# Optimization experiments

Hardware: AMD Instinct MI355X
Metric: run time of the kernel (lower is better)

Reference implementation:

```python
import jax, jax.numpy as jnp
import numpy as np

EPS = 1e-5  # BatchNorm1d default eps


def _knn_idx(coords, k):
    # squared pairwise distances via gram trick (monotone in cdist, same topk order)
    sq = jnp.sum(coords * coords, axis=-1)                     # [B,N]
    d2 = sq[:, :, None] + sq[:, None, :] - 2.0 * jnp.einsum('bnd,bmd->bnm', coords, coords)
    _, idx = jax.lax.top_k(-d2, k)                             # smallest distances
    return idx                                                  # [B,N,k]


def _shared_mlp(x, W, b, gamma, beta):
    # Linear -> BatchNorm1d (training-mode batch stats over B,N per channel) -> ReLU
    y = x @ W + b                                              # [B,N,C]
    m = jnp.mean(y, axis=(0, 1))
    v = jnp.var(y, axis=(0, 1))                                # biased, as torch BN
    y = (y - m) / jnp.sqrt(v + EPS) * gamma + beta
    return jax.nn.relu(y)


def setup_inputs() -> dict:
    key = jax.random.key(0)
    ks = jax.random.split(key, 16)
    B, N, in_ch, out_ch, k = 4, 8192, 64, 128, 16
    mid = out_ch // 2
    s = 0.05
    inp = {
        'coords': jax.random.normal(ks[0], (B, N, 3), jnp.float32),
        'feats': jax.random.normal(ks[1], (B, N, in_ch), jnp.float32),
        'k': k,
        'W1': jax.random.normal(ks[2], (in_ch, mid), jnp.float32) * s,
        'b1': jnp.zeros((mid,), jnp.float32),
        'g1': jnp.ones((mid,), jnp.float32),
        'be1': jnp.zeros((mid,), jnp.float32),
        'Wa': jax.random.normal(ks[3], (mid, mid), jnp.float32) * s,
        'ba': jnp.zeros((mid,), jnp.float32),
        'ga': jnp.ones((mid,), jnp.float32),
        'bea': jnp.zeros((mid,), jnp.float32),
        'W2': jax.random.normal(ks[4], (mid, out_ch), jnp.float32) * s,
        'b2': jnp.zeros((out_ch,), jnp.float32),
        'g2': jnp.ones((out_ch,), jnp.float32),
        'be2': jnp.zeros((out_ch,), jnp.float32),
    }
    return inp


def reference(coords, feats, k, W1, b1, g1, be1, Wa, ba, ga, bea, W2, b2, g2, be2):
    B, N, _ = coords.shape
    idx = _knn_idx(coords, k)                                  # [B,N,k]
    # gather neighbor features: feats[b, idx[b,n,j]]
    neighbors = feats[jnp.arange(B)[:, None, None], idx]       # [B,N,k,C_in]
    agg = _shared_mlp(neighbors.mean(axis=2), W1, b1, g1, be1) # [B,N,mid]
    attn = jax.nn.sigmoid(_shared_mlp(agg, Wa, ba, ga, bea))
    fused = agg * attn + agg
    return _shared_mlp(fused, W2, b2, g2, be2)                 # [B,N,out_ch]
```

## Files before the change

### kernel.cpp

```cpp
#include <hip/hip_runtime.h>
#include <hip/hip_bf16.h>
#include <hip/hip_fp16.h>
#include <math.h>

#define B_ 4
#define N_ 8192
#define K_ 16
#define BN_ (B_ * N_)
#define EPS_ 1e-5f

#define KW_ 8
#define KT_ (KW_ * 64)
#define MCAND (N_ / KW_)
#define SAMP 256
#define DEPTH 8

#define NBLK 512
#define ROWS 64

#define KEY_SENTINEL 0x7F800000FFFFFFFFULL

__global__ __launch_bounds__(256) void pack_coords(const float* __restrict__ coords,
                                                   float4* __restrict__ out) {
    int i = blockIdx.x * 256 + threadIdx.x;
    if (i >= BN_) return;
    out[i] = make_float4(coords[3 * i], coords[3 * i + 1], coords[3 * i + 2], 0.0f);
}

__global__ __launch_bounds__(256) void feats2h(const float* __restrict__ in,
                                               __half* __restrict__ outh) {
    int i = blockIdx.x * 256 + threadIdx.x;
    const float4* p = (const float4*)(in + (size_t)i * 8);
    float4 a = p[0], b = p[1];
    __half2 h0; h0.x = __float2half_rn(a.x); h0.y = __float2half_rn(a.y);
    __half2 h1; h1.x = __float2half_rn(a.z); h1.y = __float2half_rn(a.w);
    __half2 h2; h2.x = __float2half_rn(b.x); h2.y = __float2half_rn(b.y);
    __half2 h3; h3.x = __float2half_rn(b.z); h3.y = __float2half_rn(b.w);
    uint4 o;
    o.x = *(unsigned*)&h0; o.y = *(unsigned*)&h1; o.z = *(unsigned*)&h2; o.w = *(unsigned*)&h3;
    ((uint4*)outh)[i] = o;
}

__global__ __launch_bounds__(KT_) void knn_2ph(const float4* __restrict__ coords4,
                                               int* __restrict__ idxOut) {
    __shared__ unsigned long long bufp[DEPTH][KT_];
    __shared__ unsigned long long accs[KW_][64];

    int t = threadIdx.x;
    int lane = t & 63;
    int w = __builtin_amdgcn_readfirstlane(t >> 6);
    int b = blockIdx.x >> 7;
    int g = blockIdx.x & 127;

    const float4* cb = coords4 + (size_t)b * N_;
    int q = g * 64 + lane;
    float4 qc = cb[q];
    float qx = qc.x, qy = qc.y, qz = qc.z;

    const int base = w * MCAND;

    unsigned long long acc = 0;
    for (int i = 0; i < SAMP; i += 8) {
        float4 c0 = cb[base + i + 0];
        float4 c1 = cb[base + i + 1];
        float4 c2 = cb[base + i + 2];
        float4 c3 = cb[base + i + 3];
        float4 c4 = cb[base + i + 4];
        float4 c5 = cb[base + i + 5];
        float4 c6 = cb[base + i + 6];
        float4 c7 = cb[base + i + 7];
#define H1(cv)                                                         \
        {                                                              \
            float dx = qx - cv.x, dy = qy - cv.y, dz = qz - cv.z;      \
            float d2 = dx * dx;                                        \
            d2 = fmaf(dy, dy, d2);                                     \
            d2 = fmaf(dz, dz, d2);                                     \
            int e = (int)(__float_as_uint(d2) >> 23);                  \
            int bk = (e - 118) >> 1;                                   \
            bk = bk < 0 ? 0 : (bk > 7 ? 7 : bk);                       \
            acc += 1ULL << (bk << 3);                                  \
        }
        H1(c0) H1(c1) H1(c2) H1(c3) H1(c4) H1(c5) H1(c6) H1(c7)
#undef H1
    }
    accs[w][lane] = acc;
    __syncthreads();

    float T;
    {
        const unsigned long long M8 = 0x00FF00FF00FF00FFULL;
        unsigned long long se = 0, so = 0;
#pragma unroll
        for (int ww = 0; ww < KW_; ++ww) {
            unsigned long long a = accs[ww][lane];
            se += a & M8;
            so += (a >> 8) & M8;
        }
        int cum = 0;
        int B = 8;
#pragma unroll
        for (int bb = 0; bb < 8; ++bb) {
            unsigned long long s = (bb & 1) ? so : se;
            int c = (int)((s >> ((bb >> 1) << 4)) & 0xFFFF);
            cum += c;
            if (cum >= K_ && B == 8) B = bb;
        }
        T = (B >= 7) ? 3.4e38f : __uint_as_float((unsigned)(118 + 2 * B + 2) << 23);
    }

    unsigned long long key[K_];
#pragma unroll
    for (int j = 0; j < K_; j++) key[j] = KEY_SENTINEL;

    int cnt = 0;
    float limf = T;

    auto flush = [&]() {
        for (int j = 0; j < cnt; ++j) {
            unsigned long long e = bufp[j][t];
            if (e < key[K_ - 1]) {
#pragma unroll
                for (int jj = K_ - 1; jj > 0; --jj) {
                    bool up = e < key[jj - 1];
                    unsigned long long lo = (e < key[jj]) ? e : key[jj];
                    key[jj] = up ? key[jj - 1] : lo;
                }
                if (e < key[0]) key[0] = e;
            }
        }
        cnt = 0;
        float own = __uint_as_float((unsigned)(key[K_ - 1] >> 32));
        limf = fminf(own, T);
    };

    for (int i = 0; i < MCAND; i += 8) {
        float4 c0 = cb[base + i + 0];
        float4 c1 = cb[base + i + 1];
        float4 c2 = cb[base + i + 2];
        float4 c3 = cb[base + i + 3];
        float4 c4 = cb[base + i + 4];
        float4 c5 = cb[base + i + 5];
        float4 c6 = cb[base + i + 6];
        float4 c7 = cb[base + i + 7];
#define P2(cv, mm)                                                     \
        {                                                              \
            float dx = qx - cv.x, dy = qy - cv.y, dz = qz - cv.z;      \
            float d2 = dx * dx;                                        \
            d2 = fmaf(dy, dy, d2);                                     \
            d2 = fmaf(dz, dz, d2);                                     \
            if (d2 <= limf) {                                          \
                bufp[cnt][t] = ((unsigned long long)__float_as_uint(d2) << 32) | \
                               (unsigned)(mm);                         \
                cnt++;                                                 \
            }                                                          \
        }
        P2(c0, base + i + 0) P2(c1, base + i + 1) P2(c2, base + i + 2) P2(c3, base + i + 3)
        if (__any(cnt >= DEPTH - 3)) flush();
        P2(c4, base + i + 4) P2(c5, base + i + 5) P2(c6, base + i + 6) P2(c7, base + i + 7)
#undef P2
        if (__any(cnt >= DEPTH - 3)) flush();
    }
    flush();

    for (int step = 1; step < KW_; step <<= 1) {
        bool active = (w & (2 * step - 1)) == 0;
        int pb = t + step * 64;
        __syncthreads();
#pragma unroll
        for (int j = 0; j < 8; j++) bufp[j][t] = key[j];
        __syncthreads();
        if (active) {
#pragma unroll
            for (int i = 8; i < 16; i++) {
                unsigned long long o = bufp[15 - i][pb];
                key[i] = key[i] < o ? key[i] : o;
            }
        }
        __syncthreads();
#pragma unroll
        for (int j = 0; j < 8; j++) bufp[j][t] = key[8 + j];
        __syncthreads();
        if (active) {
#pragma unroll
            for (int i = 0; i < 8; i++) {
                unsigned long long o = bufp[7 - i][pb];
                key[i] = key[i] < o ? key[i] : o;
            }
#pragma unroll
            for (int s = 8; s >= 1; s >>= 1) {
#pragma unroll
                for (int i = 0; i < 16; i++) {
                    if ((i & s) == 0) {
                        unsigned long long a = key[i], c = key[i | s];
                        key[i] = a < c ? a : c;
                        key[i | s] = a < c ? c : a;
                    }
                }
            }
        }
    }

    if (w == 0) {
        int* op = idxOut + ((size_t)b * N_ + q) * K_;
#pragma unroll
        for (int r2 = 0; r2 < K_; ++r2) op[r2] = (int)(key[r2] & 0xFFFFFFFFu);
    }
}

__global__ __launch_bounds__(512) void g1_kernel(const __half* __restrict__ fh,
                                                 const int* __restrict__ idx,
                                                 const float* __restrict__ W1,
                                                 const float* __restrict__ b1,
                                                 float* __restrict__ Y1,
                                                 float* __restrict__ part1) {
    __shared__ float buf[ROWS][65];
    int t = threadIdx.x;
    int rl = t & 63;
    int h2 = __builtin_amdgcn_readfirstlane(t >> 6);
    int vbid = ((blockIdx.x & 7) << 6) + (blockIdx.x >> 3);
    int row = vbid * ROWS + rl;
    int bb = row >> 13;

    const __half* fb = fh + ((size_t)bb << 13) * 64;
    const int* ip = idx + (size_t)row * K_;

    float xh[8];
#pragma unroll
    for (int j = 0; j < 8; j++) xh[j] = 0.0f;
#pragma unroll
    for (int j = 0; j < K_; j++) {
        uint4 a = *(const uint4*)(fb + (((size_t)ip[j]) << 6) + h2 * 8);
        __half2* hp = (__half2*)&a;
#pragma unroll
        for (int p = 0; p < 4; p++) {
            float2 f = __half22float2(hp[p]);
            xh[2 * p] += f.x;
            xh[2 * p + 1] += f.y;
        }
    }
#pragma unroll
    for (int j = 0; j < 8; j++) buf[rl][h2 * 8 + j] = xh[j] * (1.0f / 16.0f);
    __syncthreads();

    float acc[8];
#pragma unroll
    for (int j = 0; j < 8; j++) acc[j] = b1[h2 * 8 + j];
#pragma unroll 1
    for (int c0 = 0; c0 < 64; c0 += 16) {
        float xr[16];
#pragma unroll
        for (int j = 0; j < 16; j++) xr[j] = buf[rl][c0 + j];
#pragma unroll
        for (int cc = 0; cc < 16; cc++) {
            float xv = xr[cc];
            const float* wr = W1 + (c0 + cc) * 64 + h2 * 8;
#pragma unroll
            for (int j = 0; j < 8; j++) acc[j] = fmaf(xv, wr[j], acc[j]);
        }
    }
    float2* yp = (float2*)(Y1 + (size_t)row * 64 + h2 * 8);
#pragma unroll
    for (int f = 0; f < 4; f++) yp[f] = make_float2(acc[2 * f], acc[2 * f + 1]);
    __syncthreads();
#pragma unroll
    for (int j = 0; j < 8; j++) buf[rl][h2 * 8 + j] = acc[j];
    __syncthreads();
    if (t < 128) {
        int c = t & 63;
        float s = 0.0f;
        if (t < 64) { for (int r = 0; r < ROWS; ++r) s += buf[r][c]; }
        else        { for (int r = 0; r < ROWS; ++r) { float v = buf[r][c]; s = fmaf(v, v, s); } }
        part1[blockIdx.x * 128 + t] = s;
    }
}

__device__ __forceinline__ void reduce_stats64(const float* __restrict__ part,
                                               const float* __restrict__ gma,
                                               const float* __restrict__ bta,
                                               float* red4, float* scs, float* shs) {
    int t = threadIdx.x;
    {
        int c = t & 127;
        int q = t >> 7;
        float s = 0.0f;
#pragma unroll 8
        for (int g = q * 128; g < q * 128 + 128; ++g) s += part[(size_t)g * 128 + c];
        red4[t] = s;
    }
    __syncthreads();
    if (t < 128) red4[t] = red4[t] + red4[t + 128] + red4[t + 256] + red4[t + 384];
    __syncthreads();
    if (t < 64) {
        float mean = red4[t] * (1.0f / BN_);
        float var = red4[t + 64] * (1.0f / BN_) - mean * mean;
        float rstd = rsqrtf(var + EPS_);
        float scl = rstd * gma[t];
        scs[t] = scl;
        shs[t] = bta[t] - mean * scl;
    }
    __syncthreads();
}

__global__ __launch_bounds__(512) void m2_kernel(const float* __restrict__ Y1,
                                                 const float* __restrict__ Wa,
                                                 const float* __restrict__ ba,
                                                 const float* __restrict__ g1,
                                                 const float* __restrict__ be1,
                                                 const float* __restrict__ part1,
                                                 float* __restrict__ X1,
                                                 float* __restrict__ Y2,
                                                 float* __restrict__ part2) {
    __shared__ float buf[ROWS][65];
    __shared__ float red4[512];
    __shared__ float scs[64], shs[64];
    int t = threadIdx.x;
    int rl = t & 63;
    int h2 = __builtin_amdgcn_readfirstlane(t >> 6);
    int row = blockIdx.x * ROWS + rl;

    reduce_stats64(part1, g1, be1, red4, scs, shs);

    const float2* y1p = (const float2*)(Y1 + (size_t)row * 64 + h2 * 8);
    float2* x1p = (float2*)(X1 + (size_t)row * 64 + h2 * 8);
#pragma unroll
    for (int f = 0; f < 4; f++) {
        float2 v = y1p[f];
        int c0 = h2 * 8 + 2 * f;
        float a = fmaxf(0.0f, fmaf(v.x, scs[c0], shs[c0]));
        float b = fmaxf(0.0f, fmaf(v.y, scs[c0 + 1], shs[c0 + 1]));
        x1p[f] = make_float2(a, b);
        buf[rl][c0] = a;
        buf[rl][c0 + 1] = b;
    }
    __syncthreads();

    float acc[8];
#pragma unroll
    for (int j = 0; j < 8; j++) acc[j] = ba[h2 * 8 + j];
#pragma unroll 1
    for (int c0 = 0; c0 < 64; c0 += 16) {
        float xr[16];
#pragma unroll
        for (int j = 0; j < 16; j++) xr[j] = buf[rl][c0 + j];
#pragma unroll
        for (int cc = 0; cc < 16; cc++) {
            float xv = xr[cc];
            const float* wr = Wa + (c0 + cc) * 64 + h2 * 8;
#pragma unroll
            for (int j = 0; j < 8; j++) acc[j] = fmaf(xv, wr[j], acc[j]);
        }
    }
    float2* y2p = (float2*)(Y2 + (size_t)row * 64 + h2 * 8);
#pragma unroll
    for (int f = 0; f < 4; f++) y2p[f] = make_float2(acc[2 * f], acc[2 * f + 1]);
    __syncthreads();
#pragma unroll
    for (int j = 0; j < 8; j++) buf[rl][h2 * 8 + j] = acc[j];
    __syncthreads();
    if (t < 128) {
        int c = t & 63;
        float s = 0.0f;
        if (t < 64) { for (int r = 0; r < ROWS; ++r) s += buf[r][c]; }
        else        { for (int r = 0; r < ROWS; ++r) { float v = buf[r][c]; s = fmaf(v, v, s); } }
        part2[blockIdx.x * 128 + t] = s;
    }
}

__global__ __launch_bounds__(512) void m3_kernel(const float* __restrict__ Y2,
                                                 const float* __restrict__ X1,
                                                 const float* __restrict__ W2,
                                                 const float* __restrict__ b2,
                                                 const float* __restrict__ ga,
                                                 const float* __restrict__ bea,
                                                 const float* __restrict__ part2,
                                                 float* __restrict__ Y3,
                                                 float* __restrict__ part3) {
    __shared__ float buf[ROWS][65];
    __shared__ float red4[512];
    __shared__ float scs[64], shs[64];
    int t = threadIdx.x;
    int rl = t & 63;
    int h2 = __builtin_amdgcn_readfirstlane(t >> 6);
    int row = blockIdx.x * ROWS + rl;

    reduce_stats64(part2, ga, bea, red4, scs, shs);

    const float2* y2p = (const float2*)(Y2 + (size_t)row * 64 + h2 * 8);
    const float2* x1p = (const float2*)(X1 + (size_t)row * 64 + h2 * 8);
#pragma unroll
    for (int f = 0; f < 4; f++) {
        float2 v = y2p[f];
        float2 u = x1p[f];
        int c0 = h2 * 8 + 2 * f;
        float t0 = fmaxf(0.0f, fmaf(v.x, scs[c0], shs[c0]));
        float t1 = fmaxf(0.0f, fmaf(v.y, scs[c0 + 1], shs[c0 + 1]));
        float a0 = 1.0f / (1.0f + __expf(-t0));
        float a1 = 1.0f / (1.0f + __expf(-t1));
        buf[rl][c0] = u.x * (1.0f + a0);
        buf[rl][c0 + 1] = u.y * (1.0f + a1);
    }
    __syncthreads();

    float acc16[16];
#pragma unroll
    for (int j = 0; j < 16; j++) acc16[j] = b2[h2 * 16 + j];
#pragma unroll 1
    for (int c0 = 0; c0 < 64; c0 += 16) {
        float xr[16];
#pragma unroll
        for (int j = 0; j < 16; j++) xr[j] = buf[rl][c0 + j];
#pragma unroll
        for (int cc = 0; cc < 16; cc++) {
            float xv = xr[cc];
            const float* wr = W2 + (c0 + cc) * 128 + h2 * 16;
#pragma unroll
            for (int j = 0; j < 16; j++) acc16[j] = fmaf(xv, wr[j], acc16[j]);
        }
    }
    float4* yp = (float4*)(Y3 + (size_t)row * 128 + h2 * 16);
#pragma unroll
    for (int f = 0; f < 4; f++)
        yp[f] = make_float4(acc16[4 * f], acc16[4 * f + 1], acc16[4 * f + 2], acc16[4 * f + 3]);

    __syncthreads();
    if (h2 < 4) {
#pragma unroll
        for (int j = 0; j < 16; j++) buf[rl][h2 * 16 + j] = acc16[j];
    }
    __syncthreads();
    if (t < 128) {
        int c = t & 63;
        float s = 0.0f;
        if (t < 64) { for (int r = 0; r < ROWS; ++r) s += buf[r][c]; }
        else        { for (int r = 0; r < ROWS; ++r) { float v = buf[r][c]; s = fmaf(v, v, s); } }
        part3[blockIdx.x * 256 + t] = s;
    }
    __syncthreads();
    if (h2 >= 4) {
#pragma unroll
        for (int j = 0; j < 16; j++) buf[rl][(h2 - 4) * 16 + j] = acc16[j];
    }
    __syncthreads();
    if (t < 128) {
        int c = t & 63;
        float s = 0.0f;
        if (t < 64) { for (int r = 0; r < ROWS; ++r) s += buf[r][c]; }
        else        { for (int r = 0; r < ROWS; ++r) { float v = buf[r][c]; s = fmaf(v, v, s); } }
        part3[blockIdx.x * 256 + 128 + t] = s;
    }
}

__global__ __launch_bounds__(256) void bnf_kernel(float* __restrict__ Y3,
                                                  const float* __restrict__ g2,
                                                  const float* __restrict__ be2,
                                                  const float* __restrict__ part3) {
    __shared__ float red[256];
    __shared__ float scs[128], shs[128];
    int t = threadIdx.x;
    {
        float s = 0.0f;
#pragma unroll 8
        for (int g = 0; g < NBLK; ++g) s += part3[(size_t)g * 256 + t];
        red[t] = s;
    }
    __syncthreads();
    if (t < 128) {
        int si = (t < 64) ? t : (t + 64);
        float mean = red[si] * (1.0f / BN_);
        float var = red[si + 64] * (1.0f / BN_) - mean * mean;
        float rstd = rsqrtf(var + EPS_);
        float scl = rstd * g2[t];
        scs[t] = scl;
        shs[t] = be2[t] - mean * scl;
    }
    __syncthreads();
    const int total = BN_ * 128 / 4;
    float4* p = (float4*)Y3;
    for (int i = blockIdx.x * 256 + t; i < total; i += 256 * 256) {
        float4 v = p[i];
        int c0 = (i * 4) & 127;
        v.x = fmaxf(0.0f, fmaf(v.x, scs[c0],     shs[c0]));
        v.y = fmaxf(0.0f, fmaf(v.y, scs[c0 + 1], shs[c0 + 1]));
        v.z = fmaxf(0.0f, fmaf(v.z, scs[c0 + 2], shs[c0 + 2]));
        v.w = fmaxf(0.0f, fmaf(v.w, scs[c0 + 3], shs[c0 + 3]));
        p[i] = v;
    }
}

extern "C" void kernel_launch(void* const* d_in, const int* in_sizes, int n_in,
                              void* d_out, int out_size, void* d_ws, size_t ws_size,
                              hipStream_t stream) {
    const float* coords = (const float*)d_in[0];
    const float* feats  = (const float*)d_in[1];
    const float* W1  = (const float*)d_in[3];
    const float* b1  = (const float*)d_in[4];
    const float* g1  = (const float*)d_in[5];
    const float* be1 = (const float*)d_in[6];
    const float* Wa  = (const float*)d_in[7];
    const float* ba  = (const float*)d_in[8];
    const float* ga  = (const float*)d_in[9];
    const float* bea = (const float*)d_in[10];
    const float* W2  = (const float*)d_in[11];
    const float* b2  = (const float*)d_in[12];
    const float* g2  = (const float*)d_in[13];
    const float* be2 = (const float*)d_in[14];

    float* ws = (float*)d_ws;
    float4* coords4 = (float4*)ws;
    int*    idxbuf  = (int*)(ws + 131072);
    __half* fh      = (__half*)(ws + 131072 + 524288);
    float*  y1 = ws + 131072 + 524288 + 1048576;
    float*  x1 = y1 + (size_t)BN_ * 64;
    float*  y2 = x1 + (size_t)BN_ * 64;
    float*  part1 = y2 + (size_t)BN_ * 64;
    float*  part2 = part1 + NBLK * 128;
    float*  part3 = part2 + NBLK * 128;
    float*  y3 = (float*)d_out;

    pack_coords<<<(BN_ + 255) / 256, 256, 0, stream>>>(coords, coords4);
    feats2h<<<BN_ * 64 / 8 / 256, 256, 0, stream>>>(feats, fh);
    knn_2ph<<<B_ * 128, KT_, 0, stream>>>(coords4, idxbuf);

    g1_kernel<<<NBLK, 512, 0, stream>>>(fh, idxbuf, W1, b1, y1, part1);
    m2_kernel<<<NBLK, 512, 0, stream>>>(y1, Wa, ba, g1, be1, part1, x1, y2, part2);
    m3_kernel<<<NBLK, 512, 0, stream>>>(y2, x1, W2, b2, ga, bea, part2, y3, part3);
    bnf_kernel<<<256, 256, 0, stream>>>(y3, g2, be2, part3);
}
```

Baseline: 279.4 us.

## Split KNN candidate scan over more warps and gate insertion on block minimum

```diff
diff --git a/kernel.cpp b/kernel.cpp
--- a/kernel.cpp
+++ b/kernel.cpp
@@ -9,10 +9,10 @@
 #define BN_ (B_ * N_)
 #define EPS_ 1e-5f
 
-#define KW_ 8
+#define KW_ 16
 #define KT_ (KW_ * 64)
 #define MCAND (N_ / KW_)
-#define SAMP 256
+#define SAMP 128
 #define DEPTH 8
 
 #define NBLK 512
@@ -142,23 +142,34 @@
         float4 c5 = cb[base + i + 5];
         float4 c6 = cb[base + i + 6];
         float4 c7 = cb[base + i + 7];
-#define P2(cv, mm)                                                     \
+        float d2a[8];
+#define DD(u, cv)                                                      \
         {                                                              \
             float dx = qx - cv.x, dy = qy - cv.y, dz = qz - cv.z;      \
             float d2 = dx * dx;                                        \
             d2 = fmaf(dy, dy, d2);                                     \
             d2 = fmaf(dz, dz, d2);                                     \
-            if (d2 <= limf) {                                          \
-                bufp[cnt][t] = ((unsigned long long)__float_as_uint(d2) << 32) | \
-                               (unsigned)(mm);                         \
-                cnt++;                                                 \
-            }                                                          \
-        }
-        P2(c0, base + i + 0) P2(c1, base + i + 1) P2(c2, base + i + 2) P2(c3, base + i + 3)
-        if (__any(cnt >= DEPTH - 3)) flush();
-        P2(c4, base + i + 4) P2(c5, base + i + 5) P2(c6, base + i + 6) P2(c7, base + i + 7)
-#undef P2
-        if (__any(cnt >= DEPTH - 3)) flush();
+            d2a[u] = d2;                                               \
+        }
+        DD(0, c0) DD(1, c1) DD(2, c2) DD(3, c3)
+        DD(4, c4) DD(5, c5) DD(6, c6) DD(7, c7)
+#undef DD
+        float m0 = fminf(d2a[0], d2a[1]);
+        float m1 = fminf(d2a[2], d2a[3]);
+        float m2 = fminf(d2a[4], d2a[5]);
+        float m3 = fminf(d2a[6], d2a[7]);
+        float minv = fminf(fminf(m0, m1), fminf(m2, m3));
+        if (__any(minv <= limf)) {
+            flush();
+#pragma unroll
+            for (int u = 0; u < 8; ++u) {
+                if (d2a[u] <= limf) {
+                    bufp[cnt][t] = ((unsigned long long)__float_as_uint(d2a[u]) << 32) |
+                                   (unsigned)(base + i + u);
+                    cnt++;
+                }
+            }
+        }
     }
     flush();
 
```

Measured after the change: 396.0 us. 1.42x slower.
